# Kernel tuning notes

Measured on AMD Instinct MI355X. Metric: run time of the kernel, lower is better.

## Reference

```python
import jax, jax.numpy as jnp
from jax import lax
import numpy as np

D_MODEL, D_STATE, D_CONV, EXPAND = 512, 16, 4, 2
D_INNER = EXPAND * D_MODEL
B_SZ, SEQ = 16, 2048


def setup_inputs() -> dict:
    key = jax.random.key(0)
    ks = jax.random.split(key, 8)
    s = 0.02
    x = jax.random.normal(ks[0], (B_SZ, SEQ, D_MODEL), jnp.float32)
    W_in = jax.random.normal(ks[1], (2 * D_INNER, D_MODEL), jnp.float32) * s
    conv_w = jax.random.normal(ks[2], (D_INNER, 1, D_CONV), jnp.float32) * s
    conv_b = jnp.zeros((D_INNER,), jnp.float32)
    W_x = jax.random.normal(ks[3], (2 * D_STATE, D_INNER), jnp.float32) * s
    W_dt = jax.random.normal(ks[4], (D_INNER, D_INNER), jnp.float32) * s
    b_dt = jnp.zeros((D_INNER,), jnp.float32)
    # A_log = -logspace(log10(0.001), log10(1.0), d_state), exactly as in source
    A_log = jnp.asarray(-np.logspace(np.log10(0.001), 0.0, D_STATE), jnp.float32)
    D = jnp.ones((D_INNER,), jnp.float32) * 0.1
    W_out = jax.random.normal(ks[5], (D_MODEL, D_INNER), jnp.float32) * s
    ln_g = jnp.ones((D_MODEL,), jnp.float32)
    ln_b = jnp.zeros((D_MODEL,), jnp.float32)
    return dict(x=x, W_in=W_in, conv_w=conv_w, conv_b=conv_b, W_x=W_x,
                W_dt=W_dt, b_dt=b_dt, A_log=A_log, D=D, W_out=W_out,
                ln_g=ln_g, ln_b=ln_b)


def _selective_scan(u, delta, A, B, C, Dp):
    # u, delta: [b, s, di]; B, C: [b, s, ds]; A: [ds]; Dp: [di]
    def step(state, inp):
        d_t, u_t, B_t, C_t = inp            # [b,di],[b,di],[b,ds],[b,ds]
        dA = jnp.exp(jnp.clip(d_t[:, :, None] * A[None, None, :], -5.0, 5.0))
        dBu = (d_t * u_t)[:, :, None] * B_t[:, None, :]
        state = dA * state + dBu            # [b,di,ds]
        y_t = jnp.einsum('bds,bs->bd', state, C_t)
        return state, y_t

    b = u.shape[0]
    init = jnp.zeros((b, D_INNER, D_STATE), u.dtype)
    xs = (delta.transpose(1, 0, 2), u.transpose(1, 0, 2),
          B.transpose(1, 0, 2), C.transpose(1, 0, 2))
    _, ys = lax.scan(step, init, xs)        # [s, b, di]
    return ys.transpose(1, 0, 2) + u * Dp


def reference(x, W_in, conv_w, conv_b, W_x, W_dt, b_dt, A_log, D, W_out, ln_g, ln_b):
    x = jnp.clip(x, -10.0, 10.0)
    x_and_res = x @ W_in.T                  # [b, s, 2*di]
    x_p, res = jnp.split(x_and_res, 2, axis=-1)
    # causal depthwise conv1d (left pad d_conv-1, truncate to seq_len)
    xc = lax.conv_general_dilated(
        x_p.transpose(0, 2, 1), conv_w, window_strides=(1,),
        padding=[(D_CONV - 1, 0)], dimension_numbers=('NCH', 'OIH', 'NCH'),
        feature_group_count=D_INNER)
    xc = (xc + conv_b[None, :, None]).transpose(0, 2, 1)  # [b, s, di]
    xc = jax.nn.silu(xc)
    ssm = xc @ W_x.T                        # [b, s, 2*ds]
    Bm, Cm = jnp.split(ssm, 2, axis=-1)
    dt = xc @ W_dt.T + b_dt                 # [b, s, di]
    y = _selective_scan(xc, dt, A_log, Bm, Cm, D)
    y = y * jax.nn.silu(res)
    out = y @ W_out.T + x
    # LayerNorm (eps=1e-5)
    mu = out.mean(-1, keepdims=True)
    var = ((out - mu) ** 2).mean(-1, keepdims=True)
    return (out - mu) * lax.rsqrt(var + 1e-5) * ln_g + ln_b
```

## Files before the change

### kernel.cpp

```cpp
#include <hip/hip_runtime.h>
#include <hip/hip_bf16.h>
#include <math.h>

#define B_SZ 16
#define SEQ 2048
#define D_MODEL 512
#define D_INNER 1024
#define D_STATE 16
#define D_CONV 4
#define NSEG 32
#define SEGLEN (SEQ / NSEG)
#define LOG2E 1.44269504f

typedef __attribute__((ext_vector_type(8))) short short8;
typedef __attribute__((ext_vector_type(4))) float f32x4;
typedef const __attribute__((address_space(1))) void* gas_ptr;
typedef __attribute__((address_space(3))) void* las_ptr;

__device__ __forceinline__ float bf2f(unsigned int bits16) {
    union { unsigned int i; float f; } v; v.i = bits16 << 16; return v.f;
}
__device__ __forceinline__ unsigned short f2bf(float f) {
    union { float f; unsigned int i; } v; v.f = f;
    unsigned int r = v.i + 0x7FFFu + ((v.i >> 16) & 1u);
    return (unsigned short)(r >> 16);
}
__device__ __forceinline__ void async_g2l(const void* g, void* l) {
    __builtin_amdgcn_global_load_lds((gas_ptr)g, (las_ptr)l, 16, 0, 0);
}
__device__ __forceinline__ float fast_exp2(float x) { return __builtin_amdgcn_exp2f(x); }
__device__ __forceinline__ float fast_rcp(float x)  { return __builtin_amdgcn_rcpf(x); }
__device__ __forceinline__ float clamp3(float x, float lo, float hi) {
    return __builtin_amdgcn_fmed3f(x, lo, hi);
}
__device__ __forceinline__ float silu(float x) {
    return x * fast_rcp(1.f + fast_exp2(-x * LOG2E));
}

__global__ __launch_bounds__(256) void cast_bf16(
    const float4* __restrict__ in, ushort4* __restrict__ out, int n4, int do_clip)
{
    int i = blockIdx.x * 256 + threadIdx.x;
    if (i >= n4) return;
    float4 v = in[i];
    if (do_clip) {
        v.x = clamp3(v.x, -10.f, 10.f);
        v.y = clamp3(v.y, -10.f, 10.f);
        v.z = clamp3(v.z, -10.f, 10.f);
        v.w = clamp3(v.w, -10.f, 10.f);
    }
    ushort4 o;
    o.x = f2bf(v.x); o.y = f2bf(v.y); o.z = f2bf(v.z); o.w = f2bf(v.w);
    out[i] = o;
}

__global__ __launch_bounds__(256) void gemm_bf16(
    const unsigned short* __restrict__ A, const unsigned short* __restrict__ Bw,
    float* __restrict__ C, int K, int ldc, int nbn_shift,
    const float* __restrict__ bias,
    const float* __restrict__ add, int ldadd, int clip_add)
{
    __shared__ unsigned short As[2][128][32];
    __shared__ unsigned short Bs[2][128][32];
    const int h = blockIdx.x;
    const int xk = h & 7;
    const int qb = h >> 3;
    const int bn = (qb & ((1 << nbn_shift) - 1)) * 128;
    const int bm = ((qb >> nbn_shift) * 8 + xk) * 128;
    const int tid = threadIdx.x;
    const int wv = tid >> 6;
    const int l  = tid & 63;
    const int lr = l >> 2;
    const int lc = l & 3;
    const int wm = (wv >> 1) * 64;
    const int wn = (wv & 1) * 64;
    const int r16 = l & 15;
    const int q   = l >> 4;
    const int gsw = (lc - ((lr >> 1) & 3)) & 3;
    const int ssw = ((q + ((r16 >> 1) & 3)) & 3) * 8;

    f32x4 acc[4][4];
    #pragma unroll
    for (int i = 0; i < 4; i++)
        #pragma unroll
        for (int j = 0; j < 4; j++)
            acc[i][j] = (f32x4){0.f, 0.f, 0.f, 0.f};

#define STAGE(kk, bb) { \
        const int k0_ = (kk) * 32; \
        _Pragma("unroll") \
        for (int p_ = 0; p_ < 2; p_++) { \
            const int row_ = wv * 32 + p_ * 16 + lr; \
            async_g2l((const char*)A + (((size_t)(bm + row_)) * K + k0_ + gsw * 8) * 2, \
                      (char*)&As[bb][0][0] + (wv * 32 + p_ * 16) * 64); \
            async_g2l((const char*)Bw + (((size_t)(bn + row_)) * K + k0_ + gsw * 8) * 2, \
                      (char*)&Bs[bb][0][0] + (wv * 32 + p_ * 16) * 64); \
        } }

    const int nk = K >> 5;
    STAGE(0, 0);
    __syncthreads();

    for (int kk = 0; kk < nk; kk++) {
        const int cur = kk & 1;
        if (kk + 1 < nk) STAGE(kk + 1, cur ^ 1);

        short8 af[4], bfv[4];
        #pragma unroll
        for (int i = 0; i < 4; i++) {
            af[i]  = *(const short8*)&As[cur][wm + i * 16 + r16][ssw];
            bfv[i] = *(const short8*)&Bs[cur][wn + i * 16 + r16][ssw];
        }
        #pragma unroll
        for (int i = 0; i < 4; i++)
            #pragma unroll
            for (int j = 0; j < 4; j++)
                acc[i][j] = __builtin_amdgcn_mfma_f32_16x16x32_bf16(
                    af[i], bfv[j], acc[i][j], 0, 0, 0);
        __syncthreads();
    }
#undef STAGE

    #pragma unroll
    for (int i = 0; i < 4; i++) {
        #pragma unroll
        for (int rr = 0; rr < 4; rr++) {
            int m = bm + wm + i * 16 + q * 4 + rr;
            #pragma unroll
            for (int j = 0; j < 4; j++) {
                int n = bn + wn + j * 16 + r16;
                float v = acc[i][j][rr];
                if (bias) v += bias[n];
                if (add) {
                    float a = add[(size_t)m * ldadd + n];
                    if (clip_add) a = clamp3(a, -10.f, 10.f);
                    v += a;
                }
                C[(size_t)m * ldc + n] = v;
            }
        }
    }
}

__global__ __launch_bounds__(256) void gemm_bc(
    const unsigned short* __restrict__ A, const unsigned short* __restrict__ Bw,
    float* __restrict__ C)
{
    const int tid = threadIdx.x;
    const int wv  = tid >> 6;
    const int l   = tid & 63;
    const int r16 = l & 15;
    const int q   = l >> 4;
    const int row0 = blockIdx.x * 64 + wv * 16;

    const unsigned short* ap  = A  + (size_t)(row0 + r16) * 1024 + q * 8;
    const unsigned short* bp0 = Bw + (size_t)r16 * 1024 + q * 8;
    const unsigned short* bp1 = Bw + (size_t)(16 + r16) * 1024 + q * 8;

    f32x4 acc0 = {0.f, 0.f, 0.f, 0.f}, acc1 = {0.f, 0.f, 0.f, 0.f};
    #pragma unroll 4
    for (int k = 0; k < 1024; k += 32) {
        short8 af = *(const short8*)(ap + k);
        short8 b0 = *(const short8*)(bp0 + k);
        short8 b1 = *(const short8*)(bp1 + k);
        acc0 = __builtin_amdgcn_mfma_f32_16x16x32_bf16(af, b0, acc0, 0, 0, 0);
        acc1 = __builtin_amdgcn_mfma_f32_16x16x32_bf16(af, b1, acc1, 0, 0, 0);
    }
    #pragma unroll
    for (int rr = 0; rr < 4; rr++) {
        int m = row0 + q * 4 + rr;
        C[(size_t)m * 32 + r16]      = acc0[rr];
        C[(size_t)m * 32 + 16 + r16] = acc1[rr];
    }
}

__global__ __launch_bounds__(256) void conv_silu(
    const float* __restrict__ xres, const float* __restrict__ cw,
    const float* __restrict__ cb, unsigned short* __restrict__ xc)
{
    int idx = blockIdx.x * 256 + threadIdx.x;
    int c4 = (idx & 255) << 2;
    int bt = idx >> 8;
    int t  = bt & (SEQ - 1);

    float4 acc = *(const float4*)(cb + c4);
    float4 w0 = *(const float4*)(cw + (c4 + 0) * 4);
    float4 w1 = *(const float4*)(cw + (c4 + 1) * 4);
    float4 w2 = *(const float4*)(cw + (c4 + 2) * 4);
    float4 w3 = *(const float4*)(cw + (c4 + 3) * 4);

    #pragma unroll
    for (int k = 0; k < D_CONV; k++) {
        int tt = t - (D_CONV - 1) + k;
        if (tt >= 0) {
            float4 xv = *(const float4*)(xres + (size_t)(bt - (D_CONV - 1) + k) * 2048 + c4);
            acc.x += xv.x * ((const float*)&w0)[k];
            acc.y += xv.y * ((const float*)&w1)[k];
            acc.z += xv.z * ((const float*)&w2)[k];
            acc.w += xv.w * ((const float*)&w3)[k];
        }
    }
    ushort4 o;
    o.x = f2bf(silu(acc.x));
    o.y = f2bf(silu(acc.y));
    o.z = f2bf(silu(acc.z));
    o.w = f2bf(silu(acc.w));
    *(ushort4*)(xc + (size_t)bt * 1024 + c4) = o;
}

__global__ __launch_bounds__(64) void scan_phaseA(
    const float* __restrict__ xres, const float* __restrict__ BC,
    const unsigned short* __restrict__ xc, const float* __restrict__ A_log,
    float* __restrict__ stA, float* __restrict__ prA)
{
    __shared__ float bc_lds[SEGLEN][32];
    const int bx = blockIdx.x;
    const int seg = bx & (NSEG - 1);
    const int dg  = (bx >> 5) & 15;
    const int b   = bx >> 9;
    if (seg == NSEG - 1) return;
    const int lane = threadIdx.x;
    const int d = dg * 64 + lane;
    const float CL = 5.f * LOG2E;

    const size_t rowbase = (size_t)b * SEQ + (size_t)seg * SEGLEN;
    const float* BCp = BC + rowbase * 32;

    #pragma unroll
    for (int c = 0; c < 8; c++)
        async_g2l(BCp + c * 256 + lane * 4,
                  (char*)&bc_lds[0][0] + c * 1024 + lane * 16);

    float A2[16];
    #pragma unroll
    for (int n = 0; n < 16; n++) A2[n] = A_log[n] * LOG2E;

    const float* dtp = xres + rowbase * 2048 + d;
    const unsigned short* up = xc + rowbase * 1024 + d;

    float st[16] = {};
    float se[16] = {};
    float dta[8], dtb[8];
    unsigned short ua[8], ub[8];

#define LOADGA(g, dt_, u_) { \
        _Pragma("unroll") for (int jj = 0; jj < 8; ++jj) { \
            const int t_ = (g) * 8 + jj; \
            dt_[jj] = dtp[(size_t)t_ * 2048]; \
            u_[jj]  = up[(size_t)t_ * 1024]; \
        } }

#define COMPGA(g, dt_, u_) { \
        _Pragma("unroll") for (int jj = 0; jj < 8; ++jj) { \
            const int t_ = (g) * 8 + jj; \
            const float dtv_ = dt_[jj]; \
            const float du_ = dtv_ * bf2f(u_[jj]); \
            float Bv_[16]; \
            _Pragma("unroll") for (int n = 0; n < 4; ++n) \
                *(float4*)&Bv_[n * 4] = *(const float4*)&bc_lds[t_][n * 4]; \
            _Pragma("unroll") for (int n = 0; n < 16; ++n) { \
                const float e_ = clamp3(dtv_ * A2[n], -CL, CL); \
                se[n] += e_; \
                st[n] = fast_exp2(e_) * st[n] + du_ * Bv_[n]; \
            } } }

    LOADGA(0, dta, ua);
    __syncthreads();

    for (int g = 0; g < 8; g += 2) {
        LOADGA(g + 1, dtb, ub);
        COMPGA(g, dta, ua);
        if (g + 2 < 8) LOADGA(g + 2, dta, ua);
        COMPGA(g + 1, dtb, ub);
    }
#undef LOADGA
#undef COMPGA

    size_t o = (((size_t)b * NSEG + seg) * 1024 + d) * 16;
    #pragma unroll
    for (int n4 = 0; n4 < 4; n4++) {
        *(float4*)(stA + o + n4 * 4) = *(float4*)&st[n4 * 4];
        float4 pv;
        pv.x = fast_exp2(clamp3(se[n4 * 4 + 0], -115.41f, 115.41f));
        pv.y = fast_exp2(clamp3(se[n4 * 4 + 1], -115.41f, 115.41f));
        pv.z = fast_exp2(clamp3(se[n4 * 4 + 2], -115.41f, 115.41f));
        pv.w = fast_exp2(clamp3(se[n4 * 4 + 3], -115.41f, 115.41f));
        *(float4*)(prA + o + n4 * 4) = pv;
    }
}

__global__ __launch_bounds__(256) void scan_combine(
    float* __restrict__ stA, const float* __restrict__ prA, int total)
{
    int idx = blockIdx.x * 256 + threadIdx.x;
    if (idx >= total) return;
    int dn = idx & 16383;
    int b  = idx >> 14;
    float prev = 0.f;
    for (int s = 0; s < NSEG; s++) {
        size_t o = ((size_t)b * NSEG + s) * 16384 + dn;
        float a = stA[o], pr = prA[o];
        stA[o] = prev;
        prev = a + pr * prev;
    }
}

__global__ __launch_bounds__(64) void scan_phaseC(
    const float* __restrict__ xres, const float* __restrict__ BC,
    const unsigned short* __restrict__ xc, const float* __restrict__ A_log,
    const float* __restrict__ Dvec, const float* __restrict__ stIn,
    unsigned short* __restrict__ y_bf)
{
    __shared__ float bc_lds[SEGLEN][32];
    const int bx = blockIdx.x;
    const int seg = bx & (NSEG - 1);
    const int dg  = (bx >> 5) & 15;
    const int b   = bx >> 9;
    const int lane = threadIdx.x;
    const int d = dg * 64 + lane;
    const float CL = 5.f * LOG2E;

    const size_t rowbase = (size_t)b * SEQ + (size_t)seg * SEGLEN;
    const float* BCp = BC + rowbase * 32;

    #pragma unroll
    for (int c = 0; c < 8; c++)
        async_g2l(BCp + c * 256 + lane * 4,
                  (char*)&bc_lds[0][0] + c * 1024 + lane * 16);

    float A2[16];
    #pragma unroll
    for (int n = 0; n < 16; n++) A2[n] = A_log[n] * LOG2E;
    const float Dp = Dvec[d];

    const float* dtp  = xres + rowbase * 2048 + d;
    const float* resp = xres + rowbase * 2048 + 1024 + d;
    const unsigned short* up = xc + rowbase * 1024 + d;
    unsigned short* yp = y_bf + rowbase * 1024 + d;

    float st[16];
    size_t o = (((size_t)b * NSEG + seg) * 1024 + d) * 16;
    #pragma unroll
    for (int n4 = 0; n4 < 4; n4++)
        *(float4*)&st[n4 * 4] = *(const float4*)(stIn + o + n4 * 4);

    float dta[8], dtb[8], ra[8], rb[8];
    unsigned short ua[8], ub[8];

#define LOADGC(g, dt_, r_, u_) { \
        _Pragma("unroll") for (int jj = 0; jj < 8; ++jj) { \
            const int t_ = (g) * 8 + jj; \
            dt_[jj] = dtp[(size_t)t_ * 2048]; \
            r_[jj]  = resp[(size_t)t_ * 2048]; \
            u_[jj]  = up[(size_t)t_ * 1024]; \
        } }

#define COMPGC(g, dt_, r_, u_) { \
        _Pragma("unroll") for (int jj = 0; jj < 8; ++jj) { \
            const int t_ = (g) * 8 + jj; \
            const float dtv_ = dt_[jj]; \
            const float uu_ = bf2f(u_[jj]); \
            const float du_ = dtv_ * uu_; \
            float Bv_[16], Cv_[16]; \
            _Pragma("unroll") for (int n = 0; n < 4; ++n) { \
                *(float4*)&Bv_[n * 4] = *(const float4*)&bc_lds[t_][n * 4]; \
                *(float4*)&Cv_[n * 4] = *(const float4*)&bc_lds[t_][16 + n * 4]; \
            } \
            float y_ = 0.f; \
            _Pragma("unroll") for (int n = 0; n < 16; ++n) { \
                const float e_ = clamp3(dtv_ * A2[n], -CL, CL); \
                st[n] = fast_exp2(e_) * st[n] + du_ * Bv_[n]; \
                y_ += st[n] * Cv_[n]; \
            } \
            const float outv_ = (y_ + uu_ * Dp) * silu(r_[jj]); \
            yp[(size_t)t_ * 1024] = f2bf(outv_); \
        } }

    LOADGC(0, dta, ra, ua);
    __syncthreads();

    for (int g = 0; g < 8; g += 2) {
        LOADGC(g + 1, dtb, rb, ub);
        COMPGC(g, dta, ra, ua);
        if (g + 2 < 8) LOADGC(g + 2, dta, ra, ua);
        COMPGC(g + 1, dtb, rb, ub);
    }
#undef LOADGC
#undef COMPGC
}

__global__ __launch_bounds__(128) void ln_kernel(
    float* __restrict__ out, const float* __restrict__ g,
    const float* __restrict__ bta)
{
    const int row = blockIdx.x;
    float* p = out + (size_t)row * D_MODEL;
    const int tid = threadIdx.x;

    float4 v = ((const float4*)p)[tid];
    float s1 = v.x + v.y + v.z + v.w;
    float s2 = v.x * v.x + v.y * v.y + v.z * v.z + v.w * v.w;
    #pragma unroll
    for (int off = 32; off > 0; off >>= 1) {
        s1 += __shfl_xor(s1, off);
        s2 += __shfl_xor(s2, off);
    }
    __shared__ float r1[2], r2[2];
    if ((tid & 63) == 0) { r1[tid >> 6] = s1; r2[tid >> 6] = s2; }
    __syncthreads();
    s1 = r1[0] + r1[1];
    s2 = r2[0] + r2[1];

    const float mu  = s1 * (1.f / D_MODEL);
    const float var = s2 * (1.f / D_MODEL) - mu * mu;
    const float rstd = rsqrtf(var + 1e-5f);

    float4 gg = ((const float4*)g)[tid];
    float4 bb = ((const float4*)bta)[tid];
    float4 o;
    o.x = (v.x - mu) * rstd * gg.x + bb.x;
    o.y = (v.y - mu) * rstd * gg.y + bb.y;
    o.z = (v.z - mu) * rstd * gg.z + bb.z;
    o.w = (v.w - mu) * rstd * gg.w + bb.w;
    ((float4*)p)[tid] = o;
}

extern "C" void kernel_launch(void* const* d_in, const int* in_sizes, int n_in,
                              void* d_out, int out_size, void* d_ws, size_t ws_size,
                              hipStream_t stream)
{
    const float* x      = (const float*)d_in[0];
    const float* W_in   = (const float*)d_in[1];
    const float* conv_w = (const float*)d_in[2];
    const float* conv_b = (const float*)d_in[3];
    const float* W_x    = (const float*)d_in[4];
    const float* W_dt   = (const float*)d_in[5];
    const float* b_dt   = (const float*)d_in[6];
    const float* A_log  = (const float*)d_in[7];
    const float* Dv     = (const float*)d_in[8];
    const float* W_out  = (const float*)d_in[9];
    const float* ln_g   = (const float*)d_in[10];
    const float* ln_b   = (const float*)d_in[11];
    float* out = (float*)d_out;

    const size_t szWin  = (size_t)2048 * 512;
    const size_t szWdt  = (size_t)1024 * 1024;
    const size_t szWout = (size_t)512 * 1024;
    const size_t szWx   = (size_t)32 * 1024;
    char* p = (char*)d_ws;
    unsigned short* Wib  = (unsigned short*)p; p += szWin * 2;
    unsigned short* Wdtb = (unsigned short*)p; p += szWdt * 2;
    unsigned short* Wob  = (unsigned short*)p; p += szWout * 2;
    unsigned short* Wxb  = (unsigned short*)p; p += szWx * 2;
    const size_t fixed_bytes = (size_t)(p - (char*)d_ws);

    const size_t per_batch =
        (size_t)SEQ * 2048 * 4
      + (size_t)SEQ * 1024 * 2
      + (size_t)SEQ * 1024 * 2
      + (size_t)SEQ * 32 * 4
      + (size_t)2 * NSEG * 1024 * 16 * 4;
    int cb = 16;
    while (cb > 1 && fixed_bytes + (size_t)cb * per_batch > ws_size) cb >>= 1;
    const int Mc = cb * SEQ;

    float*          xres  = (float*)p;          p += (size_t)Mc * 2048 * 4;
    unsigned short* ybuf  = (unsigned short*)p; p += (size_t)Mc * 1024 * 2;
    unsigned short* x_bf  = ybuf;
    unsigned short* xc_bf = (unsigned short*)p; p += (size_t)Mc * 1024 * 2;
    float*          BCb   = (float*)p;          p += (size_t)Mc * 32 * 4;
    float*          stA   = (float*)p;          p += (size_t)cb * NSEG * 16384 * 4;
    float*          prA   = (float*)p;

    cast_bf16<<<(int)(szWin / 4 + 255) / 256, 256, 0, stream>>>((const float4*)W_in,  (ushort4*)Wib,  (int)(szWin / 4), 0);
    cast_bf16<<<(int)(szWdt / 4 + 255) / 256, 256, 0, stream>>>((const float4*)W_dt,  (ushort4*)Wdtb, (int)(szWdt / 4), 0);
    cast_bf16<<<(int)(szWout / 4 + 255) / 256, 256, 0, stream>>>((const float4*)W_out, (ushort4*)Wob, (int)(szWout / 4), 0);
    cast_bf16<<<(int)(szWx / 4 + 255) / 256, 256, 0, stream>>>((const float4*)W_x,   (ushort4*)Wxb,  (int)(szWx / 4), 0);

    for (int b0 = 0; b0 < B_SZ; b0 += cb) {
        const float* xk   = x   + (size_t)b0 * SEQ * D_MODEL;
        float*       outk = out + (size_t)b0 * SEQ * D_MODEL;

        cast_bf16<<<(Mc * 512 / 4) / 256, 256, 0, stream>>>(
            (const float4*)xk, (ushort4*)x_bf, Mc * 512 / 4, 1);

        gemm_bf16<<<(2048 / 128) * (Mc / 128), 256, 0, stream>>>(
            x_bf, Wib, xres, 512, 2048, 4, nullptr, nullptr, 0, 0);

        conv_silu<<<Mc, 256, 0, stream>>>(xres, conv_w, conv_b, xc_bf);

        gemm_bc<<<Mc / 64, 256, 0, stream>>>(xc_bf, Wxb, BCb);

        gemm_bf16<<<(1024 / 128) * (Mc / 128), 256, 0, stream>>>(
            xc_bf, Wdtb, xres, 1024, 2048, 3, b_dt, nullptr, 0, 0);

        scan_phaseA<<<cb * NSEG * 16, 64, 0, stream>>>(xres, BCb, xc_bf, A_log, stA, prA);
        scan_combine<<<(cb * 16384 + 255) / 256, 256, 0, stream>>>(stA, prA, cb * 16384);
        scan_phaseC<<<cb * NSEG * 16, 64, 0, stream>>>(xres, BCb, xc_bf, A_log, Dv, stA, ybuf);

        gemm_bf16<<<(512 / 128) * (Mc / 128), 256, 0, stream>>>(
            ybuf, Wob, outk, 1024, 512, 2, nullptr, xk, 512, 1);

        ln_kernel<<<Mc, 128, 0, stream>>>(outk, ln_g, ln_b);
    }
}
```

Measured before the change: 938.7 us.

## Store in_proj and dt activations as bf16 and double scan segments

The in_proj and dt GEMMs now write bf16 instead of fp32 into the shared x/res/dt buffer, and the conv and both scan phases read bf16. This halves the traffic on the largest intermediate. The scan segment count is doubled, giving more blocks with shorter segments, and the scan kernels get an occupancy hint. Phase C reuses one register array for B and C, and the combine loop is unrolled. The risks are lower precision for dt and res, and a longer serial combine over more segments.

```diff
diff --git a/kernel.cpp b/kernel.cpp
--- a/kernel.cpp
+++ b/kernel.cpp
@@ -8,7 +8,7 @@
 #define D_INNER 1024
 #define D_STATE 16
 #define D_CONV 4
-#define NSEG 32
+#define NSEG 64
 #define SEGLEN (SEQ / NSEG)
 #define LOG2E 1.44269504f
 
@@ -56,9 +56,9 @@
 
 __global__ __launch_bounds__(256) void gemm_bf16(
     const unsigned short* __restrict__ A, const unsigned short* __restrict__ Bw,
-    float* __restrict__ C, int K, int ldc, int nbn_shift,
+    void* __restrict__ C, int K, int ldc, int nbn_shift,
     const float* __restrict__ bias,
-    const float* __restrict__ add, int ldadd, int clip_add)
+    const float* __restrict__ add, int ldadd, int clip_add, int out_bf16)
 {
     __shared__ unsigned short As[2][128][32];
     __shared__ unsigned short Bs[2][128][32];
@@ -136,7 +136,10 @@
                     if (clip_add) a = clamp3(a, -10.f, 10.f);
                     v += a;
                 }
-                C[(size_t)m * ldc + n] = v;
+                if (out_bf16)
+                    ((unsigned short*)C)[(size_t)m * ldc + n] = f2bf(v);
+                else
+                    ((float*)C)[(size_t)m * ldc + n] = v;
             }
         }
     }
@@ -175,7 +178,7 @@
 }
 
 __global__ __launch_bounds__(256) void conv_silu(
-    const float* __restrict__ xres, const float* __restrict__ cw,
+    const unsigned short* __restrict__ xp, const float* __restrict__ cw,
     const float* __restrict__ cb, unsigned short* __restrict__ xc)
 {
     int idx = blockIdx.x * 256 + threadIdx.x;
@@ -193,11 +196,11 @@
     for (int k = 0; k < D_CONV; k++) {
         int tt = t - (D_CONV - 1) + k;
         if (tt >= 0) {
-            float4 xv = *(const float4*)(xres + (size_t)(bt - (D_CONV - 1) + k) * 2048 + c4);
-            acc.x += xv.x * ((const float*)&w0)[k];
-            acc.y += xv.y * ((const float*)&w1)[k];
-            acc.z += xv.z * ((const float*)&w2)[k];
-            acc.w += xv.w * ((const float*)&w3)[k];
+            ushort4 xv = *(const ushort4*)(xp + (size_t)(bt - (D_CONV - 1) + k) * 2048 + c4);
+            acc.x += bf2f(xv.x) * ((const float*)&w0)[k];
+            acc.y += bf2f(xv.y) * ((const float*)&w1)[k];
+            acc.z += bf2f(xv.z) * ((const float*)&w2)[k];
+            acc.w += bf2f(xv.w) * ((const float*)&w3)[k];
         }
     }
     ushort4 o;
@@ -208,16 +211,16 @@
     *(ushort4*)(xc + (size_t)bt * 1024 + c4) = o;
 }
 
-__global__ __launch_bounds__(64) void scan_phaseA(
-    const float* __restrict__ xres, const float* __restrict__ BC,
+__global__ __launch_bounds__(64, 4) void scan_phaseA(
+    const unsigned short* __restrict__ xpres, const float* __restrict__ BC,
     const unsigned short* __restrict__ xc, const float* __restrict__ A_log,
     float* __restrict__ stA, float* __restrict__ prA)
 {
     __shared__ float bc_lds[SEGLEN][32];
     const int bx = blockIdx.x;
     const int seg = bx & (NSEG - 1);
-    const int dg  = (bx >> 5) & 15;
-    const int b   = bx >> 9;
+    const int dg  = (bx >> 6) & 15;
+    const int b   = bx >> 10;
     if (seg == NSEG - 1) return;
     const int lane = threadIdx.x;
     const int d = dg * 64 + lane;
@@ -227,7 +230,7 @@
     const float* BCp = BC + rowbase * 32;
 
     #pragma unroll
-    for (int c = 0; c < 8; c++)
+    for (int c = 0; c < 4; c++)
         async_g2l(BCp + c * 256 + lane * 4,
                   (char*)&bc_lds[0][0] + c * 1024 + lane * 16);
 
@@ -235,25 +238,24 @@
     #pragma unroll
     for (int n = 0; n < 16; n++) A2[n] = A_log[n] * LOG2E;
 
-    const float* dtp = xres + rowbase * 2048 + d;
-    const unsigned short* up = xc + rowbase * 1024 + d;
+    const unsigned short* dtp = xpres + rowbase * 2048 + d;
+    const unsigned short* up  = xc + rowbase * 1024 + d;
 
     float st[16] = {};
     float se[16] = {};
-    float dta[8], dtb[8];
-    unsigned short ua[8], ub[8];
+    unsigned short dta[4], dtb[4], ua[4], ub[4];
 
 #define LOADGA(g, dt_, u_) { \
-        _Pragma("unroll") for (int jj = 0; jj < 8; ++jj) { \
-            const int t_ = (g) * 8 + jj; \
+        _Pragma("unroll") for (int jj = 0; jj < 4; ++jj) { \
+            const int t_ = (g) * 4 + jj; \
             dt_[jj] = dtp[(size_t)t_ * 2048]; \
             u_[jj]  = up[(size_t)t_ * 1024]; \
         } }
 
 #define COMPGA(g, dt_, u_) { \
-        _Pragma("unroll") for (int jj = 0; jj < 8; ++jj) { \
-            const int t_ = (g) * 8 + jj; \
-            const float dtv_ = dt_[jj]; \
+        _Pragma("unroll") for (int jj = 0; jj < 4; ++jj) { \
+            const int t_ = (g) * 4 + jj; \
+            const float dtv_ = bf2f(dt_[jj]); \
             const float du_ = dtv_ * bf2f(u_[jj]); \
             float Bv_[16]; \
             _Pragma("unroll") for (int n = 0; n < 4; ++n) \
@@ -297,6 +299,7 @@
     int dn = idx & 16383;
     int b  = idx >> 14;
     float prev = 0.f;
+    #pragma unroll 4
     for (int s = 0; s < NSEG; s++) {
         size_t o = ((size_t)b * NSEG + s) * 16384 + dn;
         float a = stA[o], pr = prA[o];
@@ -305,8 +308,8 @@
     }
 }
 
-__global__ __launch_bounds__(64) void scan_phaseC(
-    const float* __restrict__ xres, const float* __restrict__ BC,
+__global__ __launch_bounds__(64, 4) void scan_phaseC(
+    const unsigned short* __restrict__ xpres, const float* __restrict__ BC,
     const unsigned short* __restrict__ xc, const float* __restrict__ A_log,
     const float* __restrict__ Dvec, const float* __restrict__ stIn,
     unsigned short* __restrict__ y_bf)
@@ -314,8 +317,8 @@
     __shared__ float bc_lds[SEGLEN][32];
     const int bx = blockIdx.x;
     const int seg = bx & (NSEG - 1);
-    const int dg  = (bx >> 5) & 15;
-    const int b   = bx >> 9;
+    const int dg  = (bx >> 6) & 15;
+    const int b   = bx >> 10;
     const int lane = threadIdx.x;
     const int d = dg * 64 + lane;
     const float CL = 5.f * LOG2E;
@@ -324,7 +327,7 @@
     const float* BCp = BC + rowbase * 32;
 
     #pragma unroll
-    for (int c = 0; c < 8; c++)
+    for (int c = 0; c < 4; c++)
         async_g2l(BCp + c * 256 + lane * 4,
                   (char*)&bc_lds[0][0] + c * 1024 + lane * 16);
 
@@ -333,9 +336,9 @@
     for (int n = 0; n < 16; n++) A2[n] = A_log[n] * LOG2E;
     const float Dp = Dvec[d];
 
-    const float* dtp  = xres + rowbase * 2048 + d;
-    const float* resp = xres + rowbase * 2048 + 1024 + d;
-    const unsigned short* up = xc + rowbase * 1024 + d;
+    const unsigned short* dtp  = xpres + rowbase * 2048 + d;
+    const unsigned short* resp = xpres + rowbase * 2048 + 1024 + d;
+    const unsigned short* up   = xc + rowbase * 1024 + d;
     unsigned short* yp = y_bf + rowbase * 1024 + d;
 
     float st[16];
@@ -344,35 +347,35 @@
     for (int n4 = 0; n4 < 4; n4++)
         *(float4*)&st[n4 * 4] = *(const float4*)(stIn + o + n4 * 4);
 
-    float dta[8], dtb[8], ra[8], rb[8];
-    unsigned short ua[8], ub[8];
+    unsigned short dta[4], dtb[4], ua[4], ub[4], ra[4], rb[4];
 
 #define LOADGC(g, dt_, r_, u_) { \
-        _Pragma("unroll") for (int jj = 0; jj < 8; ++jj) { \
-            const int t_ = (g) * 8 + jj; \
+        _Pragma("unroll") for (int jj = 0; jj < 4; ++jj) { \
+            const int t_ = (g) * 4 + jj; \
             dt_[jj] = dtp[(size_t)t_ * 2048]; \
             r_[jj]  = resp[(size_t)t_ * 2048]; \
             u_[jj]  = up[(size_t)t_ * 1024]; \
         } }
 
 #define COMPGC(g, dt_, r_, u_) { \
-        _Pragma("unroll") for (int jj = 0; jj < 8; ++jj) { \
-            const int t_ = (g) * 8 + jj; \
-            const float dtv_ = dt_[jj]; \
+        _Pragma("unroll") for (int jj = 0; jj < 4; ++jj) { \
+            const int t_ = (g) * 4 + jj; \
+            const float dtv_ = bf2f(dt_[jj]); \
             const float uu_ = bf2f(u_[jj]); \
             const float du_ = dtv_ * uu_; \
-            float Bv_[16], Cv_[16]; \
-            _Pragma("unroll") for (int n = 0; n < 4; ++n) { \
-                *(float4*)&Bv_[n * 4] = *(const float4*)&bc_lds[t_][n * 4]; \
-                *(float4*)&Cv_[n * 4] = *(const float4*)&bc_lds[t_][16 + n * 4]; \
-            } \
-            float y_ = 0.f; \
+            float V_[16]; \
+            _Pragma("unroll") for (int n = 0; n < 4; ++n) \
+                *(float4*)&V_[n * 4] = *(const float4*)&bc_lds[t_][n * 4]; \
             _Pragma("unroll") for (int n = 0; n < 16; ++n) { \
                 const float e_ = clamp3(dtv_ * A2[n], -CL, CL); \
-                st[n] = fast_exp2(e_) * st[n] + du_ * Bv_[n]; \
-                y_ += st[n] * Cv_[n]; \
+                st[n] = fast_exp2(e_) * st[n] + du_ * V_[n]; \
             } \
-            const float outv_ = (y_ + uu_ * Dp) * silu(r_[jj]); \
+            _Pragma("unroll") for (int n = 0; n < 4; ++n) \
+                *(float4*)&V_[n * 4] = *(const float4*)&bc_lds[t_][16 + n * 4]; \
+            float y_ = 0.f; \
+            _Pragma("unroll") for (int n = 0; n < 16; ++n) \
+                y_ += st[n] * V_[n]; \
+            const float outv_ = (y_ + uu_ * Dp) * silu(bf2f(r_[jj])); \
             yp[(size_t)t_ * 1024] = f2bf(outv_); \
         } }
 
@@ -455,7 +458,7 @@
     const size_t fixed_bytes = (size_t)(p - (char*)d_ws);
 
     const size_t per_batch =
-        (size_t)SEQ * 2048 * 4
+        (size_t)SEQ * 2048 * 2
       + (size_t)SEQ * 1024 * 2
       + (size_t)SEQ * 1024 * 2
       + (size_t)SEQ * 32 * 4
@@ -464,7 +467,7 @@
     while (cb > 1 && fixed_bytes + (size_t)cb * per_batch > ws_size) cb >>= 1;
     const int Mc = cb * SEQ;
 
-    float*          xres  = (float*)p;          p += (size_t)Mc * 2048 * 4;
+    unsigned short* xpres = (unsigned short*)p; p += (size_t)Mc * 2048 * 2;
     unsigned short* ybuf  = (unsigned short*)p; p += (size_t)Mc * 1024 * 2;
     unsigned short* x_bf  = ybuf;
     unsigned short* xc_bf = (unsigned short*)p; p += (size_t)Mc * 1024 * 2;
@@ -485,21 +488,21 @@
             (const float4*)xk, (ushort4*)x_bf, Mc * 512 / 4, 1);
 
         gemm_bf16<<<(2048 / 128) * (Mc / 128), 256, 0, stream>>>(
-            x_bf, Wib, xres, 512, 2048, 4, nullptr, nullptr, 0, 0);
-
-        conv_silu<<<Mc, 256, 0, stream>>>(xres, conv_w, conv_b, xc_bf);
+            x_bf, Wib, xpres, 512, 2048, 4, nullptr, nullptr, 0, 0, 1);
+
+        conv_silu<<<Mc, 256, 0, stream>>>(xpres, conv_w, conv_b, xc_bf);
 
         gemm_bc<<<Mc / 64, 256, 0, stream>>>(xc_bf, Wxb, BCb);
 
         gemm_bf16<<<(1024 / 128) * (Mc / 128), 256, 0, stream>>>(
-            xc_bf, Wdtb, xres, 1024, 2048, 3, b_dt, nullptr, 0, 0);
-
-        scan_phaseA<<<cb * NSEG * 16, 64, 0, stream>>>(xres, BCb, xc_bf, A_log, stA, prA);
+            xc_bf, Wdtb, xpres, 1024, 2048, 3, b_dt, nullptr, 0, 0, 1);
+
+        scan_phaseA<<<cb * NSEG * 16, 64, 0, stream>>>(xpres, BCb, xc_bf, A_log, stA, prA);
         scan_combine<<<(cb * 16384 + 255) / 256, 256, 0, stream>>>(stA, prA, cb * 16384);
-        scan_phaseC<<<cb * NSEG * 16, 64, 0, stream>>>(xres, BCb, xc_bf, A_log, Dv, stA, ybuf);
+        scan_phaseC<<<cb * NSEG * 16, 64, 0, stream>>>(xpres, BCb, xc_bf, A_log, Dv, stA, ybuf);
 
         gemm_bf16<<<(512 / 128) * (Mc / 128), 256, 0, stream>>>(
-            ybuf, Wob, outk, 1024, 512, 2, nullptr, xk, 512, 1);
+            ybuf, Wob, outk, 1024, 512, 2, nullptr, xk, 512, 1, 0);
 
         ln_kernel<<<Mc, 128, 0, stream>>>(outk, ln_g, ln_b);
     }
```

New measurement: 964.6 us. 2.8% more time.
